# Optimization experiments

Measured on AMD Instinct MI355X. Metric: run time of the kernel, lower is better.

Reference implementation:

```python
import jax, jax.numpy as jnp
import numpy as np

OMEGA_0 = 30.0  # SIREN frequency from init_kwargs


def setup_inputs() -> dict:
    key = jax.random.key(0)
    ks = jax.random.split(key, 8)
    B, Cin, Cout, H, L = 64, 64, 64, 128, 8192
    return {
        "x": jax.random.normal(ks[0], (B, Cin, L), dtype=jnp.float32),
        "w1": jax.random.normal(ks[1], (H, 1), dtype=jnp.float32) * (1.0 / 1.0),
        "b1": jax.random.normal(ks[2], (H,), dtype=jnp.float32) * 0.1,
        "w2": jax.random.normal(ks[3], (H, H), dtype=jnp.float32) * (1.0 / np.sqrt(H)),
        "b2": jax.random.normal(ks[4], (H,), dtype=jnp.float32) * 0.1,
        "w3": jax.random.normal(ks[5], (Cout * Cin, H), dtype=jnp.float32) * (1.0 / np.sqrt(H)),
        "b3": jax.random.normal(ks[6], (Cout * Cin,), dtype=jnp.float32) * 0.1,
        "bias": jnp.zeros((Cout,), dtype=jnp.float32),
    }


def reference(x, w1, b1, w2, b2, w3, b3, bias):
    B, Cin, L = x.shape
    Cout = bias.shape[0]
    # 1. relative positions in [-1, 1], one per input timestep
    rel = jnp.linspace(-1.0, 1.0, L)  # [L]
    # 2. SIREN kernel-generating MLP (1x1 convs over positions == per-position MLP)
    h = jnp.sin(OMEGA_0 * (rel[:, None] * w1[:, 0][None, :] + b1))       # [L, H]
    h = jnp.sin(OMEGA_0 * (h @ w2.T + b2))                               # [L, H]
    k = h @ w3.T + b3                                                    # [L, Cout*Cin]
    # torch: Kernel output [1, Cout*Cin, L].view(Cout, Cin, L)
    kernel = k.T.reshape(Cout, Cin, L)                                   # [Cout, Cin, L]
    # 3. conv1d with padding=0 and kernel length == L -> single output position
    #    (cross-correlation, exactly torch.nn.functional.conv1d)
    out = jnp.einsum("bil,oil->bo", x, kernel) + bias                    # [B, Cout]
    return out[:, :, None]                                               # [B, Cout, 1]
```

## Files before the change

### kernel.cpp

```cpp
#include <hip/hip_runtime.h>
#include <hip/hip_bf16.h>

#define LPOS 8192
#define HDIM 128
#define M_TOT 4096
#define KSPLIT 16
#define CUNITS 1024
#define BUNITS (4 * CUNITS)
#define NPART 1024

typedef float  f32x4 __attribute__((ext_vector_type(4)));
typedef short  s16x8 __attribute__((ext_vector_type(8)));
typedef unsigned int u32x4 __attribute__((ext_vector_type(4)));

__device__ __forceinline__ unsigned short bf16_rne(float f) {
    unsigned u = __builtin_bit_cast(unsigned, f);
    u += 0x7fffu + ((u >> 16) & 1u);
    return (unsigned short)(u >> 16);
}

__device__ __forceinline__ s16x8 cvt8(f32x4 a, f32x4 b) {
    s16x8 r;
    r[0] = (short)bf16_rne(a[0]); r[1] = (short)bf16_rne(a[1]);
    r[2] = (short)bf16_rne(a[2]); r[3] = (short)bf16_rne(a[3]);
    r[4] = (short)bf16_rne(b[0]); r[5] = (short)bf16_rne(b[1]);
    r[6] = (short)bf16_rne(b[2]); r[7] = (short)bf16_rne(b[3]);
    return r;
}

__device__ __forceinline__ float sum8(f32x4 a, f32x4 b) {
    return ((a[0] + a[1]) + (a[2] + a[3])) + ((b[0] + b[1]) + (b[2] + b[3]));
}

__global__ __launch_bounds__(256) void k1_siren(
        const float* __restrict__ w1, const float* __restrict__ b1,
        const float* __restrict__ w2, const float* __restrict__ b2,
        unsigned short* __restrict__ h2T) {
    __shared__ float w2sT[HDIM * 129];
    __shared__ __align__(16) float h1s[2][HDIM * 8];
    const int tid = threadIdx.x;
    const int s = tid >> 7;
    const int h = tid & 127;

    for (int idx = tid; idx < HDIM * HDIM; idx += 256)
        w2sT[(idx & 127) * 129 + (idx >> 7)] = w2[idx];

    const int l0 = blockIdx.x * 16 + s * 8;
    const float myw1 = w1[h], myb1 = b1[h];
    #pragma unroll
    for (int ls = 0; ls < 8; ++ls) {
        float rel = -1.0f + (2.0f / 8191.0f) * (float)(l0 + ls);
        h1s[s][h * 8 + ls] = __sinf(30.0f * (rel * myw1 + myb1));
    }
    __syncthreads();

    const float bb = b2[h];
    float acc[8];
    #pragma unroll
    for (int ls = 0; ls < 8; ++ls) acc[ls] = bb;

    for (int j = 0; j < HDIM; ++j) {
        float wv = w2sT[j * 129 + h];
        const f32x4* hp = (const f32x4*)&h1s[s][j * 8];
        f32x4 p0 = hp[0], p1 = hp[1];
        acc[0] += wv * p0[0]; acc[1] += wv * p0[1];
        acc[2] += wv * p0[2]; acc[3] += wv * p0[3];
        acc[4] += wv * p1[0]; acc[5] += wv * p1[1];
        acc[6] += wv * p1[2]; acc[7] += wv * p1[3];
    }

    u32x4 ov;
    #pragma unroll
    for (int q = 0; q < 4; ++q) {
        unsigned lo = bf16_rne(__sinf(30.0f * acc[2 * q]));
        unsigned hi = bf16_rne(__sinf(30.0f * acc[2 * q + 1]));
        ov[q] = lo | (hi << 16);
    }
    const size_t c = (size_t)(l0 >> 6);
    const int k8 = (l0 >> 3) & 7;
    *(u32x4*)(h2T + (c * CUNITS + (size_t)k8 * 128 + h) * 8) = ov;
}

__global__ __launch_bounds__(256, 2) void k2_fused(
        const float* __restrict__ x, const unsigned short* __restrict__ h2T,
        const float* __restrict__ w3, const float* __restrict__ b3,
        float* __restrict__ part) {
    __shared__ __align__(16) char smem[65536];
    unsigned short* lds = (unsigned short*)smem;

    const int t    = threadIdx.x;
    const int lane = t & 63;
    const int wv   = t >> 6;
    const int r    = lane & 15;
    const int kg   = lane >> 4;
    const int i    = blockIdx.x;
    const int y8   = blockIdx.y;
    const int kc   = y8 * 512;

    const float* xp = x + (size_t)((wv * 16 + r) * 64 + i) * LPOS + kc + kg * 8;

    f32x4 xr[2][4];
#define LOADX(SL, IT) do { \
        xr[SL][0] = *(const f32x4*)(xp + (IT) * 64);      \
        xr[SL][1] = *(const f32x4*)(xp + (IT) * 64 + 4);  \
        xr[SL][2] = *(const f32x4*)(xp + (IT) * 64 + 32); \
        xr[SL][3] = *(const f32x4*)(xp + (IT) * 64 + 36); \
    } while (0)

    f32x4 acc[8];
    #pragma unroll
    for (int t8 = 0; t8 < 8; ++t8) { f32x4 z = {0.f,0.f,0.f,0.f}; acc[t8] = z; }
    float sacc = 0.f;

    #pragma unroll 1
    for (int g = 0; g < 2; ++g) {
        const int base = g * 4;
        {
            const unsigned short* src = h2T + (size_t)(y8 * 2 + g) * (BUNITS * 8);
            #pragma unroll
            for (int j = 0; j < 16; ++j) {
                const int U = j * 256 + t;
                __builtin_amdgcn_global_load_lds(
                    (const unsigned int*)(src + (size_t)U * 8),
                    (unsigned int*)&lds[U * 8], 16, 0, 0);
            }
        }
        LOADX(0, base); LOADX(1, base + 1);
        __syncthreads();

        #pragma unroll
        for (int it = 0; it < 4; ++it) {
            const int sl = it & 1;
            s16x8 alo = cvt8(xr[sl][0], xr[sl][1]);
            s16x8 ahi = cvt8(xr[sl][2], xr[sl][3]);
            sacc += sum8(xr[sl][0], xr[sl][1]) + sum8(xr[sl][2], xr[sl][3]);
            if (it + 2 < 4) LOADX(sl, base + it + 2);

            #pragma unroll
            for (int t8 = 0; t8 < 8; ++t8) {
                s16x8 blo = *(const s16x8*)&lds[((size_t)it * CUNITS + kg * 128 + t8 * 16 + r) * 8];
                s16x8 bhi = *(const s16x8*)&lds[((size_t)it * CUNITS + (kg + 4) * 128 + t8 * 16 + r) * 8];
                acc[t8] = __builtin_amdgcn_mfma_f32_16x16x32_bf16(alo, blo, acc[t8], 0, 0, 0);
                acc[t8] = __builtin_amdgcn_mfma_f32_16x16x32_bf16(ahi, bhi, acc[t8], 0, 0, 0);
            }
        }
        __syncthreads();
    }
#undef LOADX

    unsigned short* As = (unsigned short*)smem;
    unsigned short* Bs = (unsigned short*)(smem + 16384);
    float* b3s = (float*)(smem + 32768);
    float* sls = (float*)(smem + 33024);

    #pragma unroll
    for (int t8 = 0; t8 < 8; ++t8) {
        const int col = t8 * 16 + r;
        const int cg = col >> 3, cw = col & 7;
        #pragma unroll
        for (int q = 0; q < 4; ++q) {
            const int b = wv * 16 + kg * 4 + q;
            As[b * 128 + ((cg ^ (b & 7)) * 8) + cw] = bf16_rne(acc[t8][q]);
        }
    }
    sacc += __shfl_xor(sacc, 16); sacc += __shfl_xor(sacc, 32);
    if (kg == 0) sls[wv * 16 + r] = sacc;

    #pragma unroll
    for (int p = 0; p < 4; ++p) {
        const int row  = p * 16 + (t >> 4);
        const int gran = t & 15;
        const float* src = w3 + (size_t)(row * 64 + i) * HDIM + gran * 8;
        f32x4 v0 = *(const f32x4*)src;
        f32x4 v1 = *(const f32x4*)(src + 4);
        *(s16x8*)&Bs[row * 128 + ((gran ^ (row & 7)) * 8)] = cvt8(v0, v1);
    }
    if (t < 64) b3s[t] = b3[t * 64 + i];
    __syncthreads();

    s16x8 bfr[4][4];
    #pragma unroll
    for (int ct = 0; ct < 4; ++ct) {
        const int o = ct * 16 + r;
        #pragma unroll
        for (int ks = 0; ks < 4; ++ks)
            bfr[ct][ks] = *(const s16x8*)&Bs[o * 128 + (((ks * 4 + kg) ^ (o & 7)) * 8)];
    }
    const int bA = wv * 16 + r;
    s16x8 af[4];
    #pragma unroll
    for (int ks = 0; ks < 4; ++ks)
        af[ks] = *(const s16x8*)&As[bA * 128 + (((ks * 4 + kg) ^ (bA & 7)) * 8)];

    f32x4 acc2[4];
    #pragma unroll
    for (int ct = 0; ct < 4; ++ct) { f32x4 z = {0.f,0.f,0.f,0.f}; acc2[ct] = z; }
    #pragma unroll
    for (int ct = 0; ct < 4; ++ct)
        #pragma unroll
        for (int ks = 0; ks < 4; ++ks)
            acc2[ct] = __builtin_amdgcn_mfma_f32_16x16x32_bf16(af[ks], bfr[ct][ks], acc2[ct], 0, 0, 0);

    float* po = part + ((size_t)i * 16 + y8) * 4096;
    #pragma unroll
    for (int ct = 0; ct < 4; ++ct) {
        const int o = ct * 16 + r;
        #pragma unroll
        for (int q = 0; q < 4; ++q) {
            const int b = wv * 16 + kg * 4 + q;
            po[b * 64 + o] = acc2[ct][q] + sls[b] * b3s[o];
        }
    }
}

__global__ __launch_bounds__(256) void k4_final(
        const float* __restrict__ part, const float* __restrict__ bias,
        float* __restrict__ out) {
    __shared__ float red[4][64];
    const int t  = threadIdx.x;
    const int il = t & 63;
    const int pg = t >> 6;
    const int idx = blockIdx.x * 64 + il;

    float s = 0.f;
    #pragma unroll 8
    for (int p = pg * 256; p < pg * 256 + 256; ++p)
        s += part[(size_t)p * 4096 + idx];
    red[pg][il] = s;
    __syncthreads();
    if (t < 64)
        out[blockIdx.x * 64 + t] = bias[t] + ((red[0][t] + red[1][t]) + (red[2][t] + red[3][t]));
}

extern "C" void kernel_launch(void* const* d_in, const int* in_sizes, int n_in,
                              void* d_out, int out_size, void* d_ws, size_t ws_size,
                              hipStream_t stream) {
    (void)in_sizes; (void)n_in; (void)out_size; (void)ws_size;
    const float* x    = (const float*)d_in[0];
    const float* w1   = (const float*)d_in[1];
    const float* b1   = (const float*)d_in[2];
    const float* w2   = (const float*)d_in[3];
    const float* b2   = (const float*)d_in[4];
    const float* w3   = (const float*)d_in[5];
    const float* b3   = (const float*)d_in[6];
    const float* bias = (const float*)d_in[7];
    float* out = (float*)d_out;

    char* ws = (char*)d_ws;
    unsigned short* h2T = (unsigned short*)ws;
    const size_t H2T_BYTES = (size_t)(LPOS / 64) * CUNITS * 16;
    float* part = (float*)(ws + H2T_BYTES);

    k1_siren<<<LPOS / 16, 256, 0, stream>>>(w1, b1, w2, b2, h2T);
    k2_fused<<<dim3(64, KSPLIT), 256, 0, stream>>>(x, h2T, w3, b3, part);
    k4_final<<<64, 256, 0, stream>>>(part, bias, out);
}
```

Baseline: 59.89 us.

## Compute SIREN hidden layer with split-bf16 MFMA instead of scalar FMA

Replaces the scalar-FP32 second SIREN layer kernel with an MFMA kernel. Both w2 and the first-layer activations are split into bf16 hi/lo parts, and three bf16 MFMAs are used to approximate fp32 accuracy. Each block handles 64 positions by 64 hidden units, computes the first layer directly into registers, and writes h2T through an LDS transpose using the same layout as before. This is meant to cut the compute cost of the 8192x128x128 matmul, at the cost of redundant first-layer sin evaluations and slightly lower precision than fp32.

```diff
diff --git a/kernel.cpp b/kernel.cpp
--- a/kernel.cpp
+++ b/kernel.cpp
@@ -18,6 +18,9 @@
     u += 0x7fffu + ((u >> 16) & 1u);
     return (unsigned short)(u >> 16);
 }
+__device__ __forceinline__ float bf16f(unsigned short v) {
+    return __builtin_bit_cast(float, (unsigned)v << 16);
+}
 
 __device__ __forceinline__ s16x8 cvt8(f32x4 a, f32x4 b) {
     s16x8 r;
@@ -32,53 +35,97 @@
     return ((a[0] + a[1]) + (a[2] + a[3])) + ((b[0] + b[1]) + (b[2] + b[3]));
 }
 
-__global__ __launch_bounds__(256) void k1_siren(
+__global__ __launch_bounds__(256) void k1_mfma(
         const float* __restrict__ w1, const float* __restrict__ b1,
         const float* __restrict__ w2, const float* __restrict__ b2,
         unsigned short* __restrict__ h2T) {
-    __shared__ float w2sT[HDIM * 129];
-    __shared__ __align__(16) float h1s[2][HDIM * 8];
-    const int tid = threadIdx.x;
-    const int s = tid >> 7;
-    const int h = tid & 127;
-
-    for (int idx = tid; idx < HDIM * HDIM; idx += 256)
-        w2sT[(idx & 127) * 129 + (idx >> 7)] = w2[idx];
-
-    const int l0 = blockIdx.x * 16 + s * 8;
-    const float myw1 = w1[h], myb1 = b1[h];
-    #pragma unroll
-    for (int ls = 0; ls < 8; ++ls) {
-        float rel = -1.0f + (2.0f / 8191.0f) * (float)(l0 + ls);
-        h1s[s][h * 8 + ls] = __sinf(30.0f * (rel * myw1 + myb1));
+    __shared__ unsigned short BsH[64 * 128];
+    __shared__ unsigned short BsL[64 * 128];
+    __shared__ unsigned short Hs[64][72];
+
+    const int t    = threadIdx.x;
+    const int lane = t & 63;
+    const int wv   = t >> 6;
+    const int r    = lane & 15;
+    const int kg   = lane >> 4;
+    const int lb   = blockIdx.x;
+    const int hh   = blockIdx.y;
+    const int l0   = lb * 64;
+
+    #pragma unroll
+    for (int p = 0; p < 4; ++p) {
+        const int row  = p * 16 + (t >> 4);
+        const int gran = t & 15;
+        const float* src = w2 + (size_t)(hh * 64 + row) * HDIM + gran * 8;
+        f32x4 v0 = *(const f32x4*)src;
+        f32x4 v1 = *(const f32x4*)(src + 4);
+        s16x8 hi = cvt8(v0, v1);
+        f32x4 e0, e1;
+        e0[0] = v0[0] - bf16f((unsigned short)hi[0]);
+        e0[1] = v0[1] - bf16f((unsigned short)hi[1]);
+        e0[2] = v0[2] - bf16f((unsigned short)hi[2]);
+        e0[3] = v0[3] - bf16f((unsigned short)hi[3]);
+        e1[0] = v1[0] - bf16f((unsigned short)hi[4]);
+        e1[1] = v1[1] - bf16f((unsigned short)hi[5]);
+        e1[2] = v1[2] - bf16f((unsigned short)hi[6]);
+        e1[3] = v1[3] - bf16f((unsigned short)hi[7]);
+        s16x8 lo = cvt8(e0, e1);
+        *(s16x8*)&BsH[row * 128 + ((gran ^ (row & 7)) * 8)] = hi;
+        *(s16x8*)&BsL[row * 128 + ((gran ^ (row & 7)) * 8)] = lo;
+    }
+
+    const int lrow = wv * 16 + r;
+    const float rel = -1.0f + (2.0f / 8191.0f) * (float)(l0 + lrow);
+    s16x8 aH[4], aL[4];
+    #pragma unroll
+    for (int ks = 0; ks < 4; ++ks) {
+        #pragma unroll
+        for (int jj = 0; jj < 8; ++jj) {
+            const int j = ks * 32 + kg * 8 + jj;
+            float v = __sinf(30.0f * (rel * w1[j] + b1[j]));
+            unsigned short hi = bf16_rne(v);
+            aH[ks][jj] = (short)hi;
+            aL[ks][jj] = (short)bf16_rne(v - bf16f(hi));
+        }
     }
     __syncthreads();
 
-    const float bb = b2[h];
-    float acc[8];
-    #pragma unroll
-    for (int ls = 0; ls < 8; ++ls) acc[ls] = bb;
-
-    for (int j = 0; j < HDIM; ++j) {
-        float wv = w2sT[j * 129 + h];
-        const f32x4* hp = (const f32x4*)&h1s[s][j * 8];
-        f32x4 p0 = hp[0], p1 = hp[1];
-        acc[0] += wv * p0[0]; acc[1] += wv * p0[1];
-        acc[2] += wv * p0[2]; acc[3] += wv * p0[3];
-        acc[4] += wv * p1[0]; acc[5] += wv * p1[1];
-        acc[6] += wv * p1[2]; acc[7] += wv * p1[3];
-    }
-
-    u32x4 ov;
-    #pragma unroll
-    for (int q = 0; q < 4; ++q) {
-        unsigned lo = bf16_rne(__sinf(30.0f * acc[2 * q]));
-        unsigned hi = bf16_rne(__sinf(30.0f * acc[2 * q + 1]));
-        ov[q] = lo | (hi << 16);
-    }
-    const size_t c = (size_t)(l0 >> 6);
-    const int k8 = (l0 >> 3) & 7;
-    *(u32x4*)(h2T + (c * CUNITS + (size_t)k8 * 128 + h) * 8) = ov;
+    f32x4 acc[4];
+    #pragma unroll
+    for (int ct = 0; ct < 4; ++ct) { f32x4 z = {0.f,0.f,0.f,0.f}; acc[ct] = z; }
+    #pragma unroll
+    for (int ct = 0; ct < 4; ++ct) {
+        const int h = ct * 16 + r;
+        #pragma unroll
+        for (int ks = 0; ks < 4; ++ks) {
+            s16x8 bh = *(const s16x8*)&BsH[h * 128 + (((ks * 4 + kg) ^ (h & 7)) * 8)];
+            s16x8 bl = *(const s16x8*)&BsL[h * 128 + (((ks * 4 + kg) ^ (h & 7)) * 8)];
+            acc[ct] = __builtin_amdgcn_mfma_f32_16x16x32_bf16(aH[ks], bh, acc[ct], 0, 0, 0);
+            acc[ct] = __builtin_amdgcn_mfma_f32_16x16x32_bf16(aH[ks], bl, acc[ct], 0, 0, 0);
+            acc[ct] = __builtin_amdgcn_mfma_f32_16x16x32_bf16(aL[ks], bh, acc[ct], 0, 0, 0);
+        }
+    }
+
+    #pragma unroll
+    for (int ct = 0; ct < 4; ++ct) {
+        const int hl = ct * 16 + r;
+        const float bb = b2[hh * 64 + hl];
+        #pragma unroll
+        for (int q = 0; q < 4; ++q) {
+            const int ll = wv * 16 + kg * 4 + q;
+            Hs[hl][ll] = bf16_rne(__sinf(30.0f * (acc[ct][q] + bb)));
+        }
+    }
+    __syncthreads();
+
+    #pragma unroll
+    for (int p = 0; p < 2; ++p) {
+        const int v  = p * 256 + t;
+        const int hl = v >> 3;
+        const int k8 = v & 7;
+        u32x4 u = *(const u32x4*)&Hs[hl][k8 * 8];
+        *(u32x4*)(h2T + ((size_t)lb * 1024 + (size_t)k8 * 128 + hh * 64 + hl) * 8) = u;
+    }
 }
 
 __global__ __launch_bounds__(256, 2) void k2_fused(
@@ -251,7 +298,7 @@
     const size_t H2T_BYTES = (size_t)(LPOS / 64) * CUNITS * 16;
     float* part = (float*)(ws + H2T_BYTES);
 
-    k1_siren<<<LPOS / 16, 256, 0, stream>>>(w1, b1, w2, b2, h2T);
+    k1_mfma<<<dim3(128, 2), 256, 0, stream>>>(w1, b1, w2, b2, h2T);
     k2_fused<<<dim3(64, KSPLIT), 256, 0, stream>>>(x, h2T, w3, b3, part);
     k4_final<<<64, 256, 0, stream>>>(part, bias, out);
 }
```

Measured after the change: 53.92 us. 1.11x faster.
